# Performance work log

Hardware: AMD Instinct MI355X
Metric: run time of the kernel (lower is better)

Reference implementation:

```python
import jax, jax.numpy as jnp
import numpy as np

B, C, H, W = 4, 64, 512, 512
NS = 2048   # n_samples edges per image
NL = 1000   # number of superpixel labels


def setup_inputs() -> dict:
    key = jax.random.key(0)
    k1, k2, k3, k4 = jax.random.split(key, 4)
    x = jax.random.normal(k1, (B, C, H, W), dtype=jnp.float32)
    label_maps = jax.random.randint(k2, (B, 1, H, W), 0, NL).astype(jnp.int32)
    edges = jax.random.randint(k3, (B, NS, 2), 0, NL).astype(jnp.int32)
    edge_weights = (jax.random.uniform(k4, (B, NS)) > 0.5).astype(jnp.float32)
    return {"x": x, "label_maps": label_maps, "edges": edges,
            "edge_weights": edge_weights, "n_labels": NL}


def reference(x, label_maps, edges, edge_weights, n_labels):
    # x: [B,C,H,W]; label_maps: [B,1,H,W] int; edges: [B,NS,2] int; edge_weights: [B,NS]
    Bd, Cd, Hd, Wd = x.shape

    def per_image_means(xi, li):
        feats = xi.reshape(Cd, Hd * Wd).T            # [HW, C]
        lab = li.reshape(-1)                          # [HW]
        sums = jax.ops.segment_sum(feats, lab, num_segments=n_labels)   # [NL, C]
        cnts = jax.ops.segment_sum(jnp.ones((Hd * Wd,), xi.dtype), lab,
                                   num_segments=n_labels)               # [NL]
        return sums / jnp.maximum(cnts, 1)[:, None]

    means = jax.vmap(per_image_means)(x, label_maps[:, 0])  # [B, NL, C]

    bi = jnp.arange(Bd)[:, None]                  # [B,1] batch index
    xa = means[bi, edges[..., 0]]                 # [B, NS, C] mean feats at edge endpoint 0
    xb = means[bi, edges[..., 1]]                 # [B, NS, C] mean feats at edge endpoint 1
    y = edge_weights[..., None]                   # [B, NS, 1] edge weight labels
    return xa, xb, y
```

## Files before the change

### kernel.cpp

```cpp
#include <hip/hip_runtime.h>

#define Bd 4
#define Cd 64
#define HWp 262144
#define NSd 2048
#define NLd 1000

#define WIN    64
#define PXW    4096
#define NBLK   (Bd * WIN)
#define NSL    8
#define CSL    8
#define PROW   8000

typedef float __attribute__((ext_vector_type(4))) floatx4;

#define OFF_PART  0
#define OFF_BCNT  (NBLK * NSL * PROW)
#define OFF_MEANS (OFF_BCNT + NBLK * NLd)
#define WS_ELEMS  (OFF_MEANS + Bd * NLd * Cd)

__device__ __forceinline__ unsigned short f2bf(float f) {
    unsigned u = __float_as_uint(f);
    u += 0x7FFFu + ((u >> 16) & 1u);
    return (unsigned short)(u >> 16);
}
__device__ __forceinline__ unsigned pack2(float lo, float hi) {
    return ((unsigned)f2bf(hi) << 16) | (unsigned)f2bf(lo);
}
__device__ __forceinline__ float bflo(unsigned u) { return __uint_as_float(u << 16); }
__device__ __forceinline__ float bfhi(unsigned u) { return __uint_as_float(u & 0xFFFF0000u); }
__device__ __forceinline__ int clampl(int l) {
    return (l < 0) ? 0 : (l >= NLd ? NLd - 1 : l);
}

__global__ __launch_bounds__(1024)
void fused_kernel(const float* __restrict__ x, const int* __restrict__ lab,
                  int* __restrict__ blockCnt, float* __restrict__ partial) {
    __shared__ int h[1024];
    __shared__ int sc[1024];
    __shared__ int cur[1024];
    __shared__ uint4 ordered[PXW];

    const int tid = threadIdx.x;
    const int g   = blockIdx.x;
    const int b   = g >> 6;
    const int win = g & 63;
    const int p0  = win * PXW;

    h[tid] = 0;
    __syncthreads();

    const int4 lv = ((const int4*)(lab + ((size_t)b << 18) + p0))[tid];
    const int l0 = clampl(lv.x), l1 = clampl(lv.y),
              l2 = clampl(lv.z), l3 = clampl(lv.w);
    atomicAdd(&h[l0], 1);
    atomicAdd(&h[l1], 1);
    atomicAdd(&h[l2], 1);
    atomicAdd(&h[l3], 1);
    __syncthreads();

    const int myCnt = h[tid];
    sc[tid] = myCnt;
    __syncthreads();
    for (int off = 1; off < 1024; off <<= 1) {
        int t = (tid >= off) ? sc[tid - off] : 0;
        __syncthreads();
        sc[tid] += t;
        __syncthreads();
    }
    const int myst = sc[tid] - myCnt;
    cur[tid] = myst;
    if (tid < NLd) blockCnt[(size_t)g * NLd + tid] = myCnt;
    __syncthreads();

    const int r0 = atomicAdd(&cur[l0], 1) & (PXW - 1);
    const int r1 = atomicAdd(&cur[l1], 1) & (PXW - 1);
    const int r2 = atomicAdd(&cur[l2], 1) & (PXW - 1);
    const int r3 = atomicAdd(&cur[l3], 1) & (PXW - 1);

    const float* __restrict__ xb = x + (((size_t)b * Cd) << 18) + p0 + 4 * tid;
    float* __restrict__ pout = partial + (size_t)g * NSL * PROW;

    floatx4 v[CSL];
    #pragma unroll
    for (int c = 0; c < CSL; ++c)
        v[c] = __builtin_nontemporal_load((const floatx4*)(xb + ((size_t)c << 18)));
    uint4 pk[4];
    #pragma unroll
    for (int j = 0; j < 4; ++j) {
        pk[j].x = pack2(v[0][j], v[1][j]);
        pk[j].y = pack2(v[2][j], v[3][j]);
        pk[j].z = pack2(v[4][j], v[5][j]);
        pk[j].w = pack2(v[6][j], v[7][j]);
    }

    for (int s = 0; s < NSL; ++s) {
        __syncthreads();
        ordered[r0] = pk[0];
        ordered[r1] = pk[1];
        ordered[r2] = pk[2];
        ordered[r3] = pk[3];
        if (s + 1 < NSL) {
            #pragma unroll
            for (int c = 0; c < CSL; ++c)
                v[c] = __builtin_nontemporal_load(
                    (const floatx4*)(xb + (((size_t)((s + 1) * CSL + c)) << 18)));
        }
        __syncthreads();

        if (tid < NLd) {
            float a0 = 0, a1 = 0, a2 = 0, a3 = 0, a4 = 0, a5 = 0, a6 = 0, a7 = 0;
            for (int i = 0; i < myCnt; ++i) {
                uint4 u = ordered[(myst + i) & (PXW - 1)];
                a0 += bflo(u.x); a1 += bfhi(u.x);
                a2 += bflo(u.y); a3 += bfhi(u.y);
                a4 += bflo(u.z); a5 += bfhi(u.z);
                a6 += bflo(u.w); a7 += bfhi(u.w);
            }
            float* dst = pout + (size_t)s * PROW + tid * 8;
            float4 o0; o0.x = a0; o0.y = a1; o0.z = a2; o0.w = a3;
            float4 o1; o1.x = a4; o1.y = a5; o1.z = a6; o1.w = a7;
            *(float4*)dst = o0;
            *(float4*)(dst + 4) = o1;
        }
        if (s + 1 < NSL) {
            #pragma unroll
            for (int j = 0; j < 4; ++j) {
                pk[j].x = pack2(v[0][j], v[1][j]);
                pk[j].y = pack2(v[2][j], v[3][j]);
                pk[j].z = pack2(v[4][j], v[5][j]);
                pk[j].w = pack2(v[6][j], v[7][j]);
            }
        }
    }
}

__global__ __launch_bounds__(256)
void combine_kernel(const float* __restrict__ partial,
                    const int* __restrict__ blockCnt,
                    float* __restrict__ means) {
    __shared__ float acc[16 * 65];
    __shared__ float ninv[16];
    const int tid = threadIdx.x;
    const int b   = blockIdx.y;
    const int l0  = blockIdx.x * 16;

    if (tid < 128) {
        float r0 = 0, r1 = 0, r2 = 0, r3 = 0, r4 = 0, r5 = 0, r6 = 0, r7 = 0;
        const float* __restrict__ pb =
            partial + (size_t)b * WIN * NSL * PROW + l0 * 8 + tid;
        for (int g = 0; g < WIN; ++g) {
            const float* __restrict__ pg = pb + (size_t)g * NSL * PROW;
            r0 += pg[0 * PROW]; r1 += pg[1 * PROW];
            r2 += pg[2 * PROW]; r3 += pg[3 * PROW];
            r4 += pg[4 * PROW]; r5 += pg[5 * PROW];
            r6 += pg[6 * PROW]; r7 += pg[7 * PROW];
        }
        const int ll = tid >> 3, j = tid & 7;
        float* a = acc + ll * 65 + j;
        a[0]  = r0; a[8]  = r1; a[16] = r2; a[24] = r3;
        a[32] = r4; a[40] = r5; a[48] = r6; a[56] = r7;
    }
    if (tid < 16) {
        int n = 0;
        for (int g = 0; g < WIN; ++g)
            n += blockCnt[(size_t)(b * WIN + g) * NLd + l0 + tid];
        ninv[tid] = 1.0f / (float)(n > 0 ? n : 1);
    }
    __syncthreads();

    const int f  = tid * 4;
    const int ll = f >> 6, c = f & 63;
    const int l  = l0 + ll;
    if (l < NLd) {
        const float sc = ninv[ll];
        const float* a = acc + ll * 65 + c;
        float4 o; o.x = a[0] * sc; o.y = a[1] * sc; o.z = a[2] * sc; o.w = a[3] * sc;
        *(float4*)(means + (((size_t)(b * NLd + l)) << 6) + c) = o;
    }
}

__global__ __launch_bounds__(256)
void gather_kernel(const float* __restrict__ means,
                   const int* __restrict__ edges,
                   const float* __restrict__ ew,
                   float* __restrict__ out) {
    const int t  = blockIdx.x * 256 + threadIdx.x;
    const int bs = t >> 6;
    const int c  = t & 63;
    const int b  = bs >> 11;

    const int la = clampl(edges[bs * 2 + 0]);
    const int lb = clampl(edges[bs * 2 + 1]);

    out[t] = means[((size_t)(b * NLd + la) << 6) + c];
    out[(size_t)Bd * NSd * Cd + t] = means[((size_t)(b * NLd + lb) << 6) + c];
    if (t < Bd * NSd)
        out[2 * (size_t)Bd * NSd * Cd + t] = ew[t];
}

#define WS_FB_ELEMS (Bd * Cd * NLd + Bd * NLd)

__global__ __launch_bounds__(256)
void fb_sums_kernel(const float* __restrict__ x, const int* __restrict__ lab,
                    float* __restrict__ sums) {
    __shared__ float lsum[NLd];
    const int tid   = threadIdx.x;
    const int chunk = blockIdx.x;
    const int c     = blockIdx.y;
    const int b     = blockIdx.z;

    for (int l = tid; l < NLd; l += 256) lsum[l] = 0.0f;
    __syncthreads();

    const float4* __restrict__ xp =
        (const float4*)x + (size_t)(b * Cd + c) * (HWp / 4);
    const int4* __restrict__ lp = (const int4*)lab + (size_t)b * (HWp / 4);

    const int nvec = HWp / 16;
    const int v0 = chunk * nvec, v1 = v0 + nvec;
    for (int v = v0 + tid; v < v1; v += 256) {
        float4 xv = xp[v];
        int4   lv = lp[v];
        atomicAdd(&lsum[clampl(lv.x)], xv.x);
        atomicAdd(&lsum[clampl(lv.y)], xv.y);
        atomicAdd(&lsum[clampl(lv.z)], xv.z);
        atomicAdd(&lsum[clampl(lv.w)], xv.w);
    }
    __syncthreads();

    float* __restrict__ dst = sums + (size_t)(b * Cd + c) * NLd;
    for (int l = tid; l < NLd; l += 256)
        atomicAdd(&dst[l], lsum[l]);
}

__global__ __launch_bounds__(256)
void fb_counts_kernel(const int* __restrict__ lab, float* __restrict__ counts) {
    __shared__ unsigned lcnt[NLd];
    const int tid   = threadIdx.x;
    const int chunk = blockIdx.x;
    const int b     = blockIdx.y;

    for (int l = tid; l < NLd; l += 256) lcnt[l] = 0u;
    __syncthreads();

    const int4* __restrict__ lp = (const int4*)lab + (size_t)b * (HWp / 4);
    const int nvec = HWp / 16;
    const int v0 = chunk * nvec, v1 = v0 + nvec;
    for (int v = v0 + tid; v < v1; v += 256) {
        int4 lv = lp[v];
        atomicAdd(&lcnt[clampl(lv.x)], 1u);
        atomicAdd(&lcnt[clampl(lv.y)], 1u);
        atomicAdd(&lcnt[clampl(lv.z)], 1u);
        atomicAdd(&lcnt[clampl(lv.w)], 1u);
    }
    __syncthreads();

    float* __restrict__ dst = counts + (size_t)b * NLd;
    for (int l = tid; l < NLd; l += 256)
        atomicAdd(&dst[l], (float)lcnt[l]);
}

__global__ __launch_bounds__(256)
void fb_gather_kernel(const float* __restrict__ sums,
                      const float* __restrict__ counts,
                      const int* __restrict__ edges,
                      const float* __restrict__ ew,
                      float* __restrict__ out) {
    const int t  = blockIdx.x * 256 + threadIdx.x;
    const int bs = t >> 6;
    const int c  = t & 63;
    const int b  = bs >> 11;

    const int la = clampl(edges[bs * 2 + 0]);
    const int lb = clampl(edges[bs * 2 + 1]);

    const float ca = fmaxf(counts[b * NLd + la], 1.0f);
    const float cb = fmaxf(counts[b * NLd + lb], 1.0f);

    const size_t plane = (size_t)(b * Cd + c) * NLd;
    out[t] = sums[plane + la] / ca;
    out[(size_t)Bd * NSd * Cd + t] = sums[plane + lb] / cb;
    if (t < Bd * NSd)
        out[2 * (size_t)Bd * NSd * Cd + t] = ew[t];
}

extern "C" void kernel_launch(void* const* d_in, const int* in_sizes, int n_in,
                              void* d_out, int out_size, void* d_ws, size_t ws_size,
                              hipStream_t stream) {
    const float* x     = (const float*)d_in[0];
    const int*   lab   = (const int*)d_in[1];
    const int*   edges = (const int*)d_in[2];
    const float* ew    = (const float*)d_in[3];
    float*       out   = (float*)d_out;

    const int n_gather = Bd * NSd * Cd;

    if (ws_size >= (size_t)WS_ELEMS * sizeof(float)) {
        float* partial  = (float*)d_ws + OFF_PART;
        int*   blockCnt = (int*)d_ws + OFF_BCNT;
        float* means    = (float*)d_ws + OFF_MEANS;

        fused_kernel<<<NBLK, 1024, 0, stream>>>(x, lab, blockCnt, partial);
        combine_kernel<<<dim3(63, Bd), 256, 0, stream>>>(partial, blockCnt, means);
        gather_kernel<<<n_gather / 256, 256, 0, stream>>>(means, edges, ew, out);
    } else {
        float* sums   = (float*)d_ws;
        float* counts = sums + (size_t)Bd * Cd * NLd;

        hipMemsetAsync(d_ws, 0, (size_t)WS_FB_ELEMS * sizeof(float), stream);

        fb_sums_kernel<<<dim3(4, Cd, Bd), 256, 0, stream>>>(x, lab, sums);
        fb_counts_kernel<<<dim3(4, Bd), 256, 0, stream>>>(lab, counts);
        fb_gather_kernel<<<n_gather / 256, 256, 0, stream>>>(sums, counts, edges, ew, out);
    }
}
```

Measured before the change: 97.56 us.

## Halve channel slice to 4 and reuse histogram for scan to cut LDS

The fused kernel now processes 4 channels per slice over 16 slices instead of 8 over 8. This halves the packed bf16 staging buffer and register arrays. The separate scan and cursor shared arrays are dropped by reusing the histogram array in place, which shrinks LDS so more 1024-thread blocks can be resident, and the launch bounds now request higher occupancy. The combine kernel is restructured so each thread reduces a float4 across windows directly, without a shared transpose. The tradeoff is twice as many slice iterations, each with its own pair of barriers and its own bucket walk over the ordered buffer.

```diff
diff --git a/kernel.cpp b/kernel.cpp
--- a/kernel.cpp
+++ b/kernel.cpp
@@ -9,9 +9,9 @@
 #define WIN    64
 #define PXW    4096
 #define NBLK   (Bd * WIN)
-#define NSL    8
-#define CSL    8
-#define PROW   8000
+#define NSL    16
+#define CSL    4
+#define PROW   4000
 
 typedef float __attribute__((ext_vector_type(4))) floatx4;
 
@@ -34,13 +34,11 @@
     return (l < 0) ? 0 : (l >= NLd ? NLd - 1 : l);
 }
 
-__global__ __launch_bounds__(1024)
+__global__ __launch_bounds__(1024, 8)
 void fused_kernel(const float* __restrict__ x, const int* __restrict__ lab,
                   int* __restrict__ blockCnt, float* __restrict__ partial) {
     __shared__ int h[1024];
-    __shared__ int sc[1024];
-    __shared__ int cur[1024];
-    __shared__ uint4 ordered[PXW];
+    __shared__ uint2 ordered[PXW];
 
     const int tid = threadIdx.x;
     const int g   = blockIdx.x;
@@ -61,77 +59,67 @@
     __syncthreads();
 
     const int myCnt = h[tid];
-    sc[tid] = myCnt;
-    __syncthreads();
+    if (tid < NLd) blockCnt[(size_t)g * NLd + tid] = myCnt;
     for (int off = 1; off < 1024; off <<= 1) {
-        int t = (tid >= off) ? sc[tid - off] : 0;
-        __syncthreads();
-        sc[tid] += t;
-        __syncthreads();
-    }
-    const int myst = sc[tid] - myCnt;
-    cur[tid] = myst;
-    if (tid < NLd) blockCnt[(size_t)g * NLd + tid] = myCnt;
-    __syncthreads();
-
-    const int r0 = atomicAdd(&cur[l0], 1) & (PXW - 1);
-    const int r1 = atomicAdd(&cur[l1], 1) & (PXW - 1);
-    const int r2 = atomicAdd(&cur[l2], 1) & (PXW - 1);
-    const int r3 = atomicAdd(&cur[l3], 1) & (PXW - 1);
+        int t = (tid >= off) ? h[tid - off] : 0;
+        __syncthreads();
+        h[tid] += t;
+        __syncthreads();
+    }
+    const int myst = h[tid] - myCnt;
+    __syncthreads();
+    h[tid] = myst;
+    __syncthreads();
+
+    const int r0 = atomicAdd(&h[l0], 1) & (PXW - 1);
+    const int r1 = atomicAdd(&h[l1], 1) & (PXW - 1);
+    const int r2 = atomicAdd(&h[l2], 1) & (PXW - 1);
+    const int r3 = atomicAdd(&h[l3], 1) & (PXW - 1);
 
     const float* __restrict__ xb = x + (((size_t)b * Cd) << 18) + p0 + 4 * tid;
     float* __restrict__ pout = partial + (size_t)g * NSL * PROW;
 
-    floatx4 v[CSL];
-    #pragma unroll
-    for (int c = 0; c < CSL; ++c)
-        v[c] = __builtin_nontemporal_load((const floatx4*)(xb + ((size_t)c << 18)));
-    uint4 pk[4];
-    #pragma unroll
-    for (int j = 0; j < 4; ++j) {
-        pk[j].x = pack2(v[0][j], v[1][j]);
-        pk[j].y = pack2(v[2][j], v[3][j]);
-        pk[j].z = pack2(v[4][j], v[5][j]);
-        pk[j].w = pack2(v[6][j], v[7][j]);
-    }
+    floatx4 v0, v1, v2, v3;
+    v0 = __builtin_nontemporal_load((const floatx4*)(xb + ((size_t)0 << 18)));
+    v1 = __builtin_nontemporal_load((const floatx4*)(xb + ((size_t)1 << 18)));
+    v2 = __builtin_nontemporal_load((const floatx4*)(xb + ((size_t)2 << 18)));
+    v3 = __builtin_nontemporal_load((const floatx4*)(xb + ((size_t)3 << 18)));
+    uint2 pk0, pk1, pk2, pk3;
+    pk0.x = pack2(v0[0], v1[0]); pk0.y = pack2(v2[0], v3[0]);
+    pk1.x = pack2(v0[1], v1[1]); pk1.y = pack2(v2[1], v3[1]);
+    pk2.x = pack2(v0[2], v1[2]); pk2.y = pack2(v2[2], v3[2]);
+    pk3.x = pack2(v0[3], v1[3]); pk3.y = pack2(v2[3], v3[3]);
 
     for (int s = 0; s < NSL; ++s) {
         __syncthreads();
-        ordered[r0] = pk[0];
-        ordered[r1] = pk[1];
-        ordered[r2] = pk[2];
-        ordered[r3] = pk[3];
+        ordered[r0] = pk0;
+        ordered[r1] = pk1;
+        ordered[r2] = pk2;
+        ordered[r3] = pk3;
         if (s + 1 < NSL) {
-            #pragma unroll
-            for (int c = 0; c < CSL; ++c)
-                v[c] = __builtin_nontemporal_load(
-                    (const floatx4*)(xb + (((size_t)((s + 1) * CSL + c)) << 18)));
+            const float* nb = xb + (((size_t)((s + 1) * CSL)) << 18);
+            v0 = __builtin_nontemporal_load((const floatx4*)(nb + ((size_t)0 << 18)));
+            v1 = __builtin_nontemporal_load((const floatx4*)(nb + ((size_t)1 << 18)));
+            v2 = __builtin_nontemporal_load((const floatx4*)(nb + ((size_t)2 << 18)));
+            v3 = __builtin_nontemporal_load((const floatx4*)(nb + ((size_t)3 << 18)));
         }
         __syncthreads();
 
         if (tid < NLd) {
-            float a0 = 0, a1 = 0, a2 = 0, a3 = 0, a4 = 0, a5 = 0, a6 = 0, a7 = 0;
+            float a0 = 0, a1 = 0, a2 = 0, a3 = 0;
             for (int i = 0; i < myCnt; ++i) {
-                uint4 u = ordered[(myst + i) & (PXW - 1)];
+                uint2 u = ordered[(myst + i) & (PXW - 1)];
                 a0 += bflo(u.x); a1 += bfhi(u.x);
                 a2 += bflo(u.y); a3 += bfhi(u.y);
-                a4 += bflo(u.z); a5 += bfhi(u.z);
-                a6 += bflo(u.w); a7 += bfhi(u.w);
             }
-            float* dst = pout + (size_t)s * PROW + tid * 8;
-            float4 o0; o0.x = a0; o0.y = a1; o0.z = a2; o0.w = a3;
-            float4 o1; o1.x = a4; o1.y = a5; o1.z = a6; o1.w = a7;
-            *(float4*)dst = o0;
-            *(float4*)(dst + 4) = o1;
+            float4 o; o.x = a0; o.y = a1; o.z = a2; o.w = a3;
+            *(float4*)(pout + (size_t)s * PROW + tid * 4) = o;
         }
         if (s + 1 < NSL) {
-            #pragma unroll
-            for (int j = 0; j < 4; ++j) {
-                pk[j].x = pack2(v[0][j], v[1][j]);
-                pk[j].y = pack2(v[2][j], v[3][j]);
-                pk[j].z = pack2(v[4][j], v[5][j]);
-                pk[j].w = pack2(v[6][j], v[7][j]);
-            }
+            pk0.x = pack2(v0[0], v1[0]); pk0.y = pack2(v2[0], v3[0]);
+            pk1.x = pack2(v0[1], v1[1]); pk1.y = pack2(v2[1], v3[1]);
+            pk2.x = pack2(v0[2], v1[2]); pk2.y = pack2(v2[2], v3[2]);
+            pk3.x = pack2(v0[3], v1[3]); pk3.y = pack2(v2[3], v3[3]);
         }
     }
 }
@@ -140,44 +128,34 @@
 void combine_kernel(const float* __restrict__ partial,
                     const int* __restrict__ blockCnt,
                     float* __restrict__ means) {
-    __shared__ float acc[16 * 65];
     __shared__ float ninv[16];
     const int tid = threadIdx.x;
     const int b   = blockIdx.y;
     const int l0  = blockIdx.x * 16;
-
-    if (tid < 128) {
-        float r0 = 0, r1 = 0, r2 = 0, r3 = 0, r4 = 0, r5 = 0, r6 = 0, r7 = 0;
-        const float* __restrict__ pb =
-            partial + (size_t)b * WIN * NSL * PROW + l0 * 8 + tid;
-        for (int g = 0; g < WIN; ++g) {
-            const float* __restrict__ pg = pb + (size_t)g * NSL * PROW;
-            r0 += pg[0 * PROW]; r1 += pg[1 * PROW];
-            r2 += pg[2 * PROW]; r3 += pg[3 * PROW];
-            r4 += pg[4 * PROW]; r5 += pg[5 * PROW];
-            r6 += pg[6 * PROW]; r7 += pg[7 * PROW];
-        }
-        const int ll = tid >> 3, j = tid & 7;
-        float* a = acc + ll * 65 + j;
-        a[0]  = r0; a[8]  = r1; a[16] = r2; a[24] = r3;
-        a[32] = r4; a[40] = r5; a[48] = r6; a[56] = r7;
-    }
+    const int s   = tid >> 4;
+    const int ll  = tid & 15;
+    const int l   = l0 + ll;
+
     if (tid < 16) {
+        const int li = (l0 + tid < NLd) ? (l0 + tid) : (NLd - 1);
         int n = 0;
         for (int g = 0; g < WIN; ++g)
-            n += blockCnt[(size_t)(b * WIN + g) * NLd + l0 + tid];
+            n += blockCnt[(size_t)(b * WIN + g) * NLd + li];
         ninv[tid] = 1.0f / (float)(n > 0 ? n : 1);
     }
     __syncthreads();
 
-    const int f  = tid * 4;
-    const int ll = f >> 6, c = f & 63;
-    const int l  = l0 + ll;
     if (l < NLd) {
+        float4 r; r.x = 0; r.y = 0; r.z = 0; r.w = 0;
+        const float* __restrict__ pb =
+            partial + (size_t)b * WIN * NSL * PROW + (size_t)s * PROW + l * 4;
+        for (int g = 0; g < WIN; ++g) {
+            float4 p = *(const float4*)(pb + (size_t)g * NSL * PROW);
+            r.x += p.x; r.y += p.y; r.z += p.z; r.w += p.w;
+        }
         const float sc = ninv[ll];
-        const float* a = acc + ll * 65 + c;
-        float4 o; o.x = a[0] * sc; o.y = a[1] * sc; o.z = a[2] * sc; o.w = a[3] * sc;
-        *(float4*)(means + (((size_t)(b * NLd + l)) << 6) + c) = o;
+        float4 o; o.x = r.x * sc; o.y = r.y * sc; o.z = r.z * sc; o.w = r.w * sc;
+        *(float4*)(means + (((size_t)(b * NLd + l)) << 6) + s * 4) = o;
     }
 }
 
```

New measurement: 86.52 us. 1.13x faster.
